# Optimization experiments

Hardware: AMD Instinct MI355X
Metric: run time of the kernel (lower is better)

Reference implementation:

```python
import jax, jax.numpy as jnp
import numpy as np
from jax import lax

SEQ, IN, H, L = 4096, 512, 2048, 2


def setup_inputs() -> dict:
    key = jax.random.key(0)
    ks = jax.random.split(key, 16)
    s = 1.0 / np.sqrt(H)  # PyTorch LSTM init scale U(-1/sqrt(H), 1/sqrt(H))
    u = lambda k, shape: jax.random.uniform(k, shape, jnp.float32, -s, s)
    return {
        "x": jax.random.normal(ks[0], (SEQ, IN), jnp.float32),
        # layer 0 (input_size -> H)
        "w_ih0": u(ks[1], (4 * H, IN)),
        "w_hh0": u(ks[2], (4 * H, H)),
        "b_ih0": u(ks[3], (4 * H,)),
        "b_hh0": u(ks[4], (4 * H,)),
        # layer 1 (H -> H)
        "w_ih1": u(ks[5], (4 * H, H)),
        "w_hh1": u(ks[6], (4 * H, H)),
        "b_ih1": u(ks[7], (4 * H,)),
        "b_hh1": u(ks[8], (4 * H,)),
        # heads: Linear(H, 1)
        "w_t": u(ks[9], (1, H)),
        "b_t": u(ks[10], (1,)),
        "w_f": u(ks[11], (1, H)),
        "b_f": u(ks[12], (1,)),
    }


def _lstm_layer(xs, w_ih, w_hh, b_ih, b_hh):
    """Single-direction LSTM over xs [T, D_in] with batch=1. PyTorch gate order i,f,g,o."""
    # Precompute input contribution for all timesteps: [T, 4H]
    gx = xs @ w_ih.T + b_ih + b_hh

    def step(carry, g_in):
        h, c = carry
        g = g_in + h @ w_hh.T  # [4H]
        i, f, gg, o = jnp.split(g, 4)
        i = jax.nn.sigmoid(i)
        f = jax.nn.sigmoid(f)
        gg = jnp.tanh(gg)
        o = jax.nn.sigmoid(o)
        c = f * c + i * gg
        h = o * jnp.tanh(c)
        return (h, c), h

    h0 = jnp.zeros((H,), xs.dtype)
    c0 = jnp.zeros((H,), xs.dtype)
    (hT, _), hs = lax.scan(step, (h0, c0), gx)
    return hs, hT  # hs: [T, H], hT: [H]


def reference(x, w_ih0, w_hh0, b_ih0, b_hh0, w_ih1, w_hh1, b_ih1, b_hh1,
              w_t, b_t, w_f, b_f):
    hs0, _ = _lstm_layer(x, w_ih0, w_hh0, b_ih0, b_hh0)
    _, hT = _lstm_layer(hs0, w_ih1, w_hh1, b_ih1, b_hh1)
    lstm_out = hT.reshape(1, 1, H)  # matches torch lstm_out of last step
    target_out = lstm_out @ w_t.T + b_t  # (1,1,1)
    feature_out = lstm_out @ w_f.T + b_f  # (1,1,1)
    return (target_out, feature_out)
```

## Files before the change

### kernel.cpp

```cpp
#include <hip/hip_runtime.h>

typedef __attribute__((ext_vector_type(4))) float f32x4;
typedef __attribute__((ext_vector_type(8))) short short8;
typedef __attribute__((ext_vector_type(2))) _Float16 half2v;
typedef unsigned int u32;
typedef unsigned short u16;
typedef unsigned long long u64;

#define T_SEQ 4096
#define HDIM  2048
#define GDIM  8192
#define INDIM 512
#define NBLK  256
#define FLAG_STRIDE 32

#if defined(__has_builtin)
#if __has_builtin(__builtin_amdgcn_fdot2)
#define HAS_FDOT2 1
#endif
#if __has_builtin(__builtin_amdgcn_exp2f)
#define EXP2F(x) __builtin_amdgcn_exp2f(x)
#endif
#endif
#ifndef HAS_FDOT2
#define HAS_FDOT2 0
#endif
#ifndef EXP2F
#define EXP2F(x) exp2f(x)
#endif

__device__ __forceinline__ u16 f2bf(float x) {
  u32 u = __float_as_uint(x);
  return (u16)((u + 0x7fffu + ((u >> 16) & 1u)) >> 16);
}
__device__ __forceinline__ u16 f2h(float x) {
  _Float16 h = (_Float16)x;
  return __builtin_bit_cast(unsigned short, h);
}
__device__ __forceinline__ float hlo(u32 u) {
  return (float)__builtin_bit_cast(_Float16, (unsigned short)(u & 0xffffu));
}
__device__ __forceinline__ float hhi(u32 u) {
  return (float)__builtin_bit_cast(_Float16, (unsigned short)(u >> 16));
}

__device__ __forceinline__ int aload(const int* p) {
  return __hip_atomic_load(p, __ATOMIC_RELAXED, __HIP_MEMORY_SCOPE_AGENT);
}
__device__ __forceinline__ void astore(int* p, int v) {
  __hip_atomic_store(p, v, __ATOMIC_RELAXED, __HIP_MEMORY_SCOPE_AGENT);
}
__device__ __forceinline__ u64 aload64(const u64* p) {
  return __hip_atomic_load(p, __ATOMIC_RELAXED, __HIP_MEMORY_SCOPE_AGENT);
}
__device__ __forceinline__ void astoref(float* p, float v) {
  __hip_atomic_store(p, v, __ATOMIC_RELAXED, __HIP_MEMORY_SCOPE_AGENT);
}

__global__ void k_zero_f32(float* __restrict__ p, int n) {
  int i = blockIdx.x * blockDim.x + threadIdx.x;
  int st = gridDim.x * blockDim.x;
  for (; i < n; i += st) p[i] = 0.f;
}

__global__ void k_bias_sum(const float* __restrict__ a, const float* __restrict__ b,
                           float* __restrict__ o, int n) {
  int i = blockIdx.x * blockDim.x + threadIdx.x;
  if (i < n) o[i] = a[i] + b[i];
}

__global__ void k_cvt_bf16(const float* __restrict__ in, u16* __restrict__ out, int n) {
  int i = blockIdx.x * blockDim.x + threadIdx.x;
  int st = gridDim.x * blockDim.x;
  for (; i < n; i += st) out[i] = f2bf(in[i]);
}

__global__ __launch_bounds__(512) void k_prep_whh(const float* __restrict__ w,
                                                  uint4* __restrict__ out) {
  const int bid = blockIdx.x;
  const int tid = threadIdx.x;
#pragma unroll
  for (int s = 0; s < 16; ++s) {
    int slot = s * 512 + tid;
    int l = slot & 63, r3 = slot >> 6;
    int g = r3 & 3, q = (r3 >> 2) & 3, wv = r3 >> 4;
    int grow = q * HDIM + bid * 8 + wv;
    const float* src = w + (size_t)grow * HDIM + l * 32 + g * 8;
    uint4 o;
    o.x = (u32)f2h(src[0]) | ((u32)f2h(src[1]) << 16);
    o.y = (u32)f2h(src[2]) | ((u32)f2h(src[3]) << 16);
    o.z = (u32)f2h(src[4]) | ((u32)f2h(src[5]) << 16);
    o.w = (u32)f2h(src[6]) | ((u32)f2h(src[7]) << 16);
    out[((size_t)bid * 16 + s) * 512 + tid] = o;
  }
}

template <bool AF32>
__global__ __launch_bounds__(256) void gemm_bt_bias(
    const void* __restrict__ Av, const u16* __restrict__ B,
    const float* __restrict__ bias, float* __restrict__ C,
    int M, int N, int K)
{
  __shared__ u16 As[128 * 64];
  __shared__ u16 Bs[128 * 64];
  const int tid = threadIdx.x;
  const int m0 = blockIdx.y * 128;
  const int n0 = blockIdx.x * 128;
  const int w = tid >> 6;
  const int lane = tid & 63;
  const int wm = (w >> 1) * 64, wn = (w & 1) * 64;
  const int lr = lane & 15, lk = lane >> 4;

  f32x4 acc[4][4];
  f32x4 zero = {0.f, 0.f, 0.f, 0.f};
#pragma unroll
  for (int i = 0; i < 4; ++i)
#pragma unroll
    for (int j = 0; j < 4; ++j) acc[i][j] = zero;

  const int r = tid >> 1;
  const int sbase = (tid & 1) * 4;

  for (int kt = 0; kt < K; kt += 64) {
    uint4 va[4], vb[4];
#pragma unroll
    for (int s = 0; s < 4; ++s) {
      if constexpr (AF32) {
        const float* ga = (const float*)Av + (size_t)(m0 + r) * K + kt + (sbase + s) * 8;
        float4 f0 = *reinterpret_cast<const float4*>(ga);
        float4 f1 = *reinterpret_cast<const float4*>(ga + 4);
        va[s].x = (u32)f2bf(f0.x) | ((u32)f2bf(f0.y) << 16);
        va[s].y = (u32)f2bf(f0.z) | ((u32)f2bf(f0.w) << 16);
        va[s].z = (u32)f2bf(f1.x) | ((u32)f2bf(f1.y) << 16);
        va[s].w = (u32)f2bf(f1.z) | ((u32)f2bf(f1.w) << 16);
      } else {
        const u16* ga = (const u16*)Av + (size_t)(m0 + r) * K + kt + (sbase + s) * 8;
        va[s] = *reinterpret_cast<const uint4*>(ga);
      }
      const u16* gb = B + (size_t)(n0 + r) * K + kt + (sbase + s) * 8;
      vb[s] = *reinterpret_cast<const uint4*>(gb);
    }
    __syncthreads();
#pragma unroll
    for (int s = 0; s < 4; ++s) {
      int ps = (sbase + s) ^ (r & 7);
      *reinterpret_cast<uint4*>(&As[r * 64 + ps * 8]) = va[s];
      *reinterpret_cast<uint4*>(&Bs[r * 64 + ps * 8]) = vb[s];
    }
    __syncthreads();
#pragma unroll
    for (int k32 = 0; k32 < 2; ++k32) {
      short8 af[4], bg[4];
#pragma unroll
      for (int i = 0; i < 4; ++i) {
        int arow = wm + i * 16 + lr;
        int aslot = (k32 * 4 + lk) ^ (arow & 7);
        af[i] = *reinterpret_cast<const short8*>(&As[arow * 64 + aslot * 8]);
        int brow = wn + i * 16 + lr;
        int bslot = (k32 * 4 + lk) ^ (brow & 7);
        bg[i] = *reinterpret_cast<const short8*>(&Bs[brow * 64 + bslot * 8]);
      }
#pragma unroll
      for (int i = 0; i < 4; ++i)
#pragma unroll
        for (int j = 0; j < 4; ++j)
          acc[i][j] = __builtin_amdgcn_mfma_f32_16x16x32_bf16(af[i], bg[j], acc[i][j], 0, 0, 0);
    }
  }

#pragma unroll
  for (int j = 0; j < 4; ++j) {
    int gcol = n0 + wn + j * 16 + lr;
    float bv = bias[gcol];
#pragma unroll
    for (int i = 0; i < 4; ++i) {
      int grow = m0 + wm + i * 16 + lk * 4;
#pragma unroll
      for (int rr = 0; rr < 4; ++rr)
        C[(size_t)(grow + rr) * N + gcol] = acc[i][j][rr] + bv;
    }
  }
}

__global__ __launch_bounds__(512, 1) void lstm_rec(
    const float* __restrict__ gx,
    const uint4* __restrict__ wp,
    float* __restrict__ hhist,
    int* __restrict__ flags,
    int hmask, int T)
{
  __shared__ uint4 wlds[16 * 512];
  __shared__ float4 hT[512];
  const int tid = threadIdx.x;
  const int bid = blockIdx.x;
  const int wv = tid >> 6;
  const int l = tid & 63;

#pragma unroll
  for (int s = 0; s < 16; ++s)
    wlds[s * 512 + tid] = wp[((size_t)bid * 16 + s) * 512 + tid];
  __syncthreads();

  float c = 0.f;

  for (int t = 0; t < T; ++t) {
    uint4 wr[16];
#pragma unroll
    for (int s = 0; s < 16; ++s) wr[s] = wlds[(wv * 16 + s) * 64 + l];
#pragma unroll
    for (int s = 0; s < 16; ++s)
      asm volatile("" : "+v"(wr[s].x), "+v"(wr[s].y), "+v"(wr[s].z), "+v"(wr[s].w));

    float gv = 0.f;
    if (l < 4) gv = gx[(size_t)t * GDIM + l * HDIM + bid * 8 + wv];

    if (wv == 0) {
      const int* f0 = &flags[(l * 4 + 0) * FLAG_STRIDE];
      const int* f1 = &flags[(l * 4 + 1) * FLAG_STRIDE];
      const int* f2 = &flags[(l * 4 + 2) * FLAG_STRIDE];
      const int* f3 = &flags[(l * 4 + 3) * FLAG_STRIDE];
      while (true) {
        int m0 = min(min(aload(f0), aload(f1)), min(aload(f2), aload(f3)));
        if (__all(m0 >= t)) break;
        __builtin_amdgcn_s_sleep(1);
      }
    }
    __syncthreads();

    {
      const u64* hsrc = (const u64*)(hhist + (size_t)(t & hmask) * HDIM);
      u64 d0 = aload64(&hsrc[tid * 2]);
      u64 d1 = aload64(&hsrc[tid * 2 + 1]);
      float4 hv;
      hv.x = __uint_as_float((u32)d0);
      hv.y = __uint_as_float((u32)(d0 >> 32));
      hv.z = __uint_as_float((u32)d1);
      hv.w = __uint_as_float((u32)(d1 >> 32));
      int G2 = tid & 7, sb = tid >> 3;
      hT[G2 * 64 + (sb ^ ((G2 * 9) & 63))] = hv;
    }
    __syncthreads();

    float a0 = 0.f, a1 = 0.f, a2 = 0.f, a3 = 0.f;
#pragma unroll
    for (int g = 0; g < 4; ++g) {
      const int G0 = g * 2, G1 = g * 2 + 1;
      float4 h0 = hT[G0 * 64 + (l ^ ((G0 * 9) & 63))];
      float4 h1 = hT[G1 * 64 + (l ^ ((G1 * 9) & 63))];
#if HAS_FDOT2
      half2v p0, p1, p2, p3;
      p0[0] = (_Float16)h0.x; p0[1] = (_Float16)h0.y;
      p1[0] = (_Float16)h0.z; p1[1] = (_Float16)h0.w;
      p2[0] = (_Float16)h1.x; p2[1] = (_Float16)h1.y;
      p3[0] = (_Float16)h1.z; p3[1] = (_Float16)h1.w;
#define FD2(wu, pp, acc) __builtin_amdgcn_fdot2(__builtin_bit_cast(half2v, (wu)), (pp), (acc), false)
      a0 = FD2(wr[0 + g].x, p0, FD2(wr[0 + g].y, p1, FD2(wr[0 + g].z, p2, FD2(wr[0 + g].w, p3, a0))));
      a1 = FD2(wr[4 + g].x, p0, FD2(wr[4 + g].y, p1, FD2(wr[4 + g].z, p2, FD2(wr[4 + g].w, p3, a1))));
      a2 = FD2(wr[8 + g].x, p0, FD2(wr[8 + g].y, p1, FD2(wr[8 + g].z, p2, FD2(wr[8 + g].w, p3, a2))));
      a3 = FD2(wr[12 + g].x, p0, FD2(wr[12 + g].y, p1, FD2(wr[12 + g].z, p2, FD2(wr[12 + g].w, p3, a3))));
#undef FD2
#else
      a0 += hlo(wr[0 + g].x) * h0.x + hhi(wr[0 + g].x) * h0.y + hlo(wr[0 + g].y) * h0.z + hhi(wr[0 + g].y) * h0.w +
            hlo(wr[0 + g].z) * h1.x + hhi(wr[0 + g].z) * h1.y + hlo(wr[0 + g].w) * h1.z + hhi(wr[0 + g].w) * h1.w;
      a1 += hlo(wr[4 + g].x) * h0.x + hhi(wr[4 + g].x) * h0.y + hlo(wr[4 + g].y) * h0.z + hhi(wr[4 + g].y) * h0.w +
            hlo(wr[4 + g].z) * h1.x + hhi(wr[4 + g].z) * h1.y + hlo(wr[4 + g].w) * h1.z + hhi(wr[4 + g].w) * h1.w;
      a2 += hlo(wr[8 + g].x) * h0.x + hhi(wr[8 + g].x) * h0.y + hlo(wr[8 + g].y) * h0.z + hhi(wr[8 + g].y) * h0.w +
            hlo(wr[8 + g].z) * h1.x + hhi(wr[8 + g].z) * h1.y + hlo(wr[8 + g].w) * h1.z + hhi(wr[8 + g].w) * h1.w;
      a3 += hlo(wr[12 + g].x) * h0.x + hhi(wr[12 + g].x) * h0.y + hlo(wr[12 + g].y) * h0.z + hhi(wr[12 + g].y) * h0.w +
            hlo(wr[12 + g].z) * h1.x + hhi(wr[12 + g].z) * h1.y + hlo(wr[12 + g].w) * h1.z + hhi(wr[12 + g].w) * h1.w;
#endif
    }
#pragma unroll
    for (int m = 32; m >= 1; m >>= 1) {
      a0 += __shfl_xor(a0, m);
      a1 += __shfl_xor(a1, m);
      a2 += __shfl_xor(a2, m);
      a3 += __shfl_xor(a3, m);
    }
    float g0 = __shfl(gv, 0), g1 = __shfl(gv, 1), g2 = __shfl(gv, 2), g3 = __shfl(gv, 3);

    {
      const float L2E = 1.44269504f;
      float pre = (l & 2) ? ((l & 1) ? a3 + g3 : a2 + g2)
                          : ((l & 1) ? a1 + g1 : a0 + g0);
      float k = (l == 2) ? 2.f * L2E : -L2E;
      float e = EXP2F(k * pre);
      float act = (l == 2) ? (1.f - 2.f / (e + 1.f)) : (1.f / (1.f + e));
      float i_ = __shfl(act, 0);
      float f_ = __shfl(act, 1);
      float gg = __shfl(act, 2);
      float o_ = __shfl(act, 3);
      c = f_ * c + i_ * gg;
      float th = 1.f - 2.f / (EXP2F(2.f * L2E * c) + 1.f);
      float hval = o_ * th;
      if (l == 0) {
        astoref(&hhist[(size_t)((t + 1) & hmask) * HDIM + bid * 8 + wv], hval);
      }
    }
    __syncthreads();
    if (tid == 0) astore(&flags[bid * FLAG_STRIDE], t + 1);
  }
}

__global__ void k_heads(const float* __restrict__ h, const float* __restrict__ wt,
                        const float* __restrict__ bt, const float* __restrict__ wf,
                        const float* __restrict__ bfp, float* __restrict__ out) {
  int tid = threadIdx.x;
  float st = 0.f, sf = 0.f;
  for (int i = tid; i < HDIM; i += 256) {
    float hv = h[i];
    st += hv * wt[i];
    sf += hv * wf[i];
  }
#pragma unroll
  for (int m = 32; m >= 1; m >>= 1) {
    st += __shfl_xor(st, m, 64);
    sf += __shfl_xor(sf, m, 64);
  }
  __shared__ float ra[4], rb[4];
  if ((tid & 63) == 0) { ra[tid >> 6] = st; rb[tid >> 6] = sf; }
  __syncthreads();
  if (tid == 0) {
    out[0] = ra[0] + ra[1] + ra[2] + ra[3] + bt[0];
    out[1] = rb[0] + rb[1] + rb[2] + rb[3] + bfp[0];
  }
}

extern "C" void kernel_launch(void* const* d_in, const int* in_sizes, int n_in,
                              void* d_out, int out_size, void* d_ws, size_t ws_size,
                              hipStream_t stream) {
  const float* x     = (const float*)d_in[0];
  const float* w_ih0 = (const float*)d_in[1];
  const float* w_hh0 = (const float*)d_in[2];
  const float* b_ih0 = (const float*)d_in[3];
  const float* b_hh0 = (const float*)d_in[4];
  const float* w_ih1 = (const float*)d_in[5];
  const float* w_hh1 = (const float*)d_in[6];
  const float* b_ih1 = (const float*)d_in[7];
  const float* b_hh1 = (const float*)d_in[8];
  const float* w_t   = (const float*)d_in[9];
  const float* b_t   = (const float*)d_in[10];
  const float* w_f   = (const float*)d_in[11];
  const float* b_f   = (const float*)d_in[12];

  char* p = (char*)d_ws;
  float* gx    = (float*)(p);
  float* hs0f  = (float*)(p + 134217728);
  u16*   xb    = (u16*)  (p + 167780352);
  u16*   wb0   = (u16*)  (p + 171974656);
  u16*   wb1   = (u16*)  (p + 180363264);
  uint4* wprep = (uint4*)(p + 213917696);
  float* h1r   = (float*)(p + 247472128);
  float* bias0 = (float*)(p + 247504896);
  float* bias1 = (float*)(p + 247537664);
  int*   flags0= (int*)  (p + 247570432);
  int*   flags1= (int*)  (p + 247603200);

  k_zero_f32<<<8, 256, 0, stream>>>(hs0f, HDIM);
  k_zero_f32<<<32, 256, 0, stream>>>(h1r, 4 * HDIM);
  k_zero_f32<<<64, 256, 0, stream>>>((float*)flags0, 2 * NBLK * FLAG_STRIDE);
  k_bias_sum<<<GDIM / 256, 256, 0, stream>>>(b_ih0, b_hh0, bias0, GDIM);
  k_bias_sum<<<GDIM / 256, 256, 0, stream>>>(b_ih1, b_hh1, bias1, GDIM);
  k_cvt_bf16<<<1024, 256, 0, stream>>>(x, xb, T_SEQ * INDIM);
  k_cvt_bf16<<<1024, 256, 0, stream>>>(w_ih0, wb0, GDIM * INDIM);
  k_cvt_bf16<<<2048, 256, 0, stream>>>(w_ih1, wb1, GDIM * HDIM);

  k_prep_whh<<<NBLK, 512, 0, stream>>>(w_hh0, wprep);
  gemm_bt_bias<false><<<dim3(GDIM / 128, T_SEQ / 128), 256, 0, stream>>>(
      xb, wb0, bias0, gx, T_SEQ, GDIM, INDIM);
  lstm_rec<<<NBLK, 512, 0, stream>>>(gx, wprep, hs0f, flags0, 0x7fffffff, T_SEQ);

  gemm_bt_bias<true><<<dim3(GDIM / 128, T_SEQ / 128), 256, 0, stream>>>(
      hs0f + HDIM, wb1, bias1, gx, T_SEQ, GDIM, HDIM);
  k_prep_whh<<<NBLK, 512, 0, stream>>>(w_hh1, wprep);
  lstm_rec<<<NBLK, 512, 0, stream>>>(gx, wprep, h1r, flags1, 3, T_SEQ);

  k_heads<<<1, 256, 0, stream>>>(h1r + (size_t)(T_SEQ & 3) * HDIM, w_t, b_t, w_f, b_f,
                                 (float*)d_out);
}
```

Measured before the change: 23.56 ms.

## Replace flag-based step barrier with tagged h publication in low mantissa bits

Removes the separate per-block flag store and poll followed by a second h load. Each block now publishes its hidden values into a 4-slot ring, one cache line per block, with a 2-bit epoch tag stored in the low mantissa bits of each float. Consumers spin directly on the data until the tags match, so the wait and the data fetch become a single round trip. LDS h buffers are double-buffered, which lets one __syncthreads per step be dropped. The cost is a tiny precision loss in h from overwriting mantissa bits, plus more polling traffic from wave 0.

```diff
diff --git a/kernel.cpp b/kernel.cpp
--- a/kernel.cpp
+++ b/kernel.cpp
@@ -12,7 +12,7 @@
 #define GDIM  8192
 #define INDIM 512
 #define NBLK  256
-#define FLAG_STRIDE 32
+#define LINE_U64 16
 
 #if defined(__has_builtin)
 #if __has_builtin(__builtin_amdgcn_fdot2)
@@ -44,23 +44,29 @@
   return (float)__builtin_bit_cast(_Float16, (unsigned short)(u >> 16));
 }
 
-__device__ __forceinline__ int aload(const int* p) {
-  return __hip_atomic_load(p, __ATOMIC_RELAXED, __HIP_MEMORY_SCOPE_AGENT);
-}
-__device__ __forceinline__ void astore(int* p, int v) {
-  __hip_atomic_store(p, v, __ATOMIC_RELAXED, __HIP_MEMORY_SCOPE_AGENT);
-}
 __device__ __forceinline__ u64 aload64(const u64* p) {
   return __hip_atomic_load(p, __ATOMIC_RELAXED, __HIP_MEMORY_SCOPE_AGENT);
 }
-__device__ __forceinline__ void astoref(float* p, float v) {
+__device__ __forceinline__ void astore64(u64* p, u64 v) {
   __hip_atomic_store(p, v, __ATOMIC_RELAXED, __HIP_MEMORY_SCOPE_AGENT);
+}
+__device__ __forceinline__ bool tagok(u64 x, u32 tg) {
+  return (((u32)x & 3u) == tg) && (((u32)(x >> 32) & 3u) == tg);
 }
 
 __global__ void k_zero_f32(float* __restrict__ p, int n) {
   int i = blockIdx.x * blockDim.x + threadIdx.x;
   int st = gridDim.x * blockDim.x;
   for (; i < n; i += st) p[i] = 0.f;
+}
+
+__global__ void k_init_hpub(u64* __restrict__ a, u64* __restrict__ b) {
+  int i = blockIdx.x * blockDim.x + threadIdx.x;
+  if (i < 4 * NBLK * LINE_U64) {
+    u64 v = (i < NBLK * LINE_U64) ? 0x0000000100000001ULL : 0ULL;
+    a[i] = v;
+    b[i] = v;
+  }
 }
 
 __global__ void k_bias_sum(const float* __restrict__ a, const float* __restrict__ b,
@@ -182,15 +188,18 @@
   }
 }
 
-__global__ __launch_bounds__(512, 1) void lstm_rec(
+__global__ __launch_bounds__(512, 1)
+__attribute__((amdgpu_waves_per_eu(2, 2)))
+void lstm_rec(
     const float* __restrict__ gx,
     const uint4* __restrict__ wp,
-    float* __restrict__ hhist,
-    int* __restrict__ flags,
-    int hmask, int T)
+    u64* __restrict__ hpub,
+    float* __restrict__ hist,
+    int T)
 {
   __shared__ uint4 wlds[16 * 512];
-  __shared__ float4 hT[512];
+  __shared__ float4 hT2[2][512];
+  __shared__ float h_out[8];
   const int tid = threadIdx.x;
   const int bid = blockIdx.x;
   const int wv = tid >> 6;
@@ -215,29 +224,37 @@
     if (l < 4) gv = gx[(size_t)t * GDIM + l * HDIM + bid * 8 + wv];
 
     if (wv == 0) {
-      const int* f0 = &flags[(l * 4 + 0) * FLAG_STRIDE];
-      const int* f1 = &flags[(l * 4 + 1) * FLAG_STRIDE];
-      const int* f2 = &flags[(l * 4 + 2) * FLAG_STRIDE];
-      const int* f3 = &flags[(l * 4 + 3) * FLAG_STRIDE];
-      while (true) {
-        int m0 = min(min(aload(f0), aload(f1)), min(aload(f2), aload(f3)));
-        if (__all(m0 >= t)) break;
-        __builtin_amdgcn_s_sleep(1);
+      const u32 tg = (((u32)t >> 2) + 1) & 3u;
+      const u64* base = hpub + (size_t)(t & 3) * (NBLK * LINE_U64);
+      u64 d[16];
+      u32 done = 0;
+      while (done != 0xFu) {
+#pragma unroll
+        for (int pi = 0; pi < 4; ++pi) {
+          if (done & (1u << pi)) continue;
+          const u64* ln = base + (size_t)(l * 4 + pi) * LINE_U64;
+          u64 x0 = aload64(ln + 0);
+          u64 x1 = aload64(ln + 1);
+          u64 x2 = aload64(ln + 2);
+          u64 x3 = aload64(ln + 3);
+          if (tagok(x0, tg) && tagok(x1, tg) && tagok(x2, tg) && tagok(x3, tg)) {
+            d[pi * 4 + 0] = x0; d[pi * 4 + 1] = x1;
+            d[pi * 4 + 2] = x2; d[pi * 4 + 3] = x3;
+            done |= (1u << pi);
+          }
+        }
+        if (done != 0xFu) __builtin_amdgcn_s_sleep(1);
       }
-    }
-    __syncthreads();
-
-    {
-      const u64* hsrc = (const u64*)(hhist + (size_t)(t & hmask) * HDIM);
-      u64 d0 = aload64(&hsrc[tid * 2]);
-      u64 d1 = aload64(&hsrc[tid * 2 + 1]);
-      float4 hv;
-      hv.x = __uint_as_float((u32)d0);
-      hv.y = __uint_as_float((u32)(d0 >> 32));
-      hv.z = __uint_as_float((u32)d1);
-      hv.w = __uint_as_float((u32)(d1 >> 32));
-      int G2 = tid & 7, sb = tid >> 3;
-      hT[G2 * 64 + (sb ^ ((G2 * 9) & 63))] = hv;
+#pragma unroll
+      for (int j = 0; j < 8; ++j) {
+        u64 a = d[2 * j], b = d[2 * j + 1];
+        float4 hv;
+        hv.x = __uint_as_float((u32)a);
+        hv.y = __uint_as_float((u32)(a >> 32));
+        hv.z = __uint_as_float((u32)b);
+        hv.w = __uint_as_float((u32)(b >> 32));
+        hT2[t & 1][j * 64 + (l ^ ((j * 9) & 63))] = hv;
+      }
     }
     __syncthreads();
 
@@ -245,8 +262,8 @@
 #pragma unroll
     for (int g = 0; g < 4; ++g) {
       const int G0 = g * 2, G1 = g * 2 + 1;
-      float4 h0 = hT[G0 * 64 + (l ^ ((G0 * 9) & 63))];
-      float4 h1 = hT[G1 * 64 + (l ^ ((G1 * 9) & 63))];
+      float4 h0 = hT2[t & 1][G0 * 64 + (l ^ ((G0 * 9) & 63))];
+      float4 h1 = hT2[t & 1][G1 * 64 + (l ^ ((G1 * 9) & 63))];
 #if HAS_FDOT2
       half2v p0, p1, p2, p3;
       p0[0] = (_Float16)h0.x; p0[1] = (_Float16)h0.y;
@@ -292,23 +309,34 @@
       float o_ = __shfl(act, 3);
       c = f_ * c + i_ * gg;
       float th = 1.f - 2.f / (EXP2F(2.f * L2E * c) + 1.f);
-      float hval = o_ * th;
-      if (l == 0) {
-        astoref(&hhist[(size_t)((t + 1) & hmask) * HDIM + bid * 8 + wv], hval);
+      if (l == 0) h_out[wv] = o_ * th;
+    }
+    __syncthreads();
+
+    if (wv == 4 && l < 4) {
+      const u32 tg1 = (((u32)(t + 1) >> 2) + 1) & 3u;
+      float ha = h_out[2 * l], hb = h_out[2 * l + 1];
+      u32 ba = (__float_as_uint(ha) & ~3u) | tg1;
+      u32 bb = (__float_as_uint(hb) & ~3u) | tg1;
+      astore64(hpub + (size_t)((t + 1) & 3) * (NBLK * LINE_U64) + bid * LINE_U64 + l,
+               (u64)ba | ((u64)bb << 32));
+      if (hist) {
+        float2 hv2; hv2.x = ha; hv2.y = hb;
+        *reinterpret_cast<float2*>(hist + (size_t)(t + 1) * HDIM + bid * 8 + 2 * l) = hv2;
       }
     }
-    __syncthreads();
-    if (tid == 0) astore(&flags[bid * FLAG_STRIDE], t + 1);
-  }
-}
-
-__global__ void k_heads(const float* __restrict__ h, const float* __restrict__ wt,
+  }
+}
+
+__global__ void k_heads(const u64* __restrict__ hp, const float* __restrict__ wt,
                         const float* __restrict__ bt, const float* __restrict__ wf,
                         const float* __restrict__ bfp, float* __restrict__ out) {
   int tid = threadIdx.x;
   float st = 0.f, sf = 0.f;
   for (int i = tid; i < HDIM; i += 256) {
-    float hv = h[i];
+    u64 wpair = hp[(size_t)(i >> 3) * LINE_U64 + ((i & 7) >> 1)];
+    float hv = (i & 1) ? __uint_as_float((u32)(wpair >> 32))
+                       : __uint_as_float((u32)wpair);
     st += hv * wt[i];
     sf += hv * wf[i];
   }
@@ -350,15 +378,13 @@
   u16*   wb0   = (u16*)  (p + 171974656);
   u16*   wb1   = (u16*)  (p + 180363264);
   uint4* wprep = (uint4*)(p + 213917696);
-  float* h1r   = (float*)(p + 247472128);
-  float* bias0 = (float*)(p + 247504896);
-  float* bias1 = (float*)(p + 247537664);
-  int*   flags0= (int*)  (p + 247570432);
-  int*   flags1= (int*)  (p + 247603200);
+  u64*   hpub0 = (u64*)  (p + 247472128);
+  u64*   hpub1 = (u64*)  (p + 247603200);
+  float* bias0 = (float*)(p + 247734272);
+  float* bias1 = (float*)(p + 247767040);
 
   k_zero_f32<<<8, 256, 0, stream>>>(hs0f, HDIM);
-  k_zero_f32<<<32, 256, 0, stream>>>(h1r, 4 * HDIM);
-  k_zero_f32<<<64, 256, 0, stream>>>((float*)flags0, 2 * NBLK * FLAG_STRIDE);
+  k_init_hpub<<<64, 256, 0, stream>>>(hpub0, hpub1);
   k_bias_sum<<<GDIM / 256, 256, 0, stream>>>(b_ih0, b_hh0, bias0, GDIM);
   k_bias_sum<<<GDIM / 256, 256, 0, stream>>>(b_ih1, b_hh1, bias1, GDIM);
   k_cvt_bf16<<<1024, 256, 0, stream>>>(x, xb, T_SEQ * INDIM);
@@ -368,13 +394,13 @@
   k_prep_whh<<<NBLK, 512, 0, stream>>>(w_hh0, wprep);
   gemm_bt_bias<false><<<dim3(GDIM / 128, T_SEQ / 128), 256, 0, stream>>>(
       xb, wb0, bias0, gx, T_SEQ, GDIM, INDIM);
-  lstm_rec<<<NBLK, 512, 0, stream>>>(gx, wprep, hs0f, flags0, 0x7fffffff, T_SEQ);
+  lstm_rec<<<NBLK, 512, 0, stream>>>(gx, wprep, hpub0, hs0f, T_SEQ);
 
   gemm_bt_bias<true><<<dim3(GDIM / 128, T_SEQ / 128), 256, 0, stream>>>(
       hs0f + HDIM, wb1, bias1, gx, T_SEQ, GDIM, HDIM);
   k_prep_whh<<<NBLK, 512, 0, stream>>>(w_hh1, wprep);
-  lstm_rec<<<NBLK, 512, 0, stream>>>(gx, wprep, h1r, flags1, 3, T_SEQ);
-
-  k_heads<<<1, 256, 0, stream>>>(h1r + (size_t)(T_SEQ & 3) * HDIM, w_t, b_t, w_f, b_f,
-                                 (float*)d_out);
-}
+  lstm_rec<<<NBLK, 512, 0, stream>>>(gx, wprep, hpub1, (float*)nullptr, T_SEQ);
+
+  k_heads<<<1, 256, 0, stream>>>(hpub1 + (size_t)(T_SEQ & 3) * (NBLK * LINE_U64),
+                                 w_t, b_t, w_f, b_f, (float*)d_out);
+}
```

Result: slower. 35.12 ms (+49.1%).

## Replace per-block flag barrier with per-wave byte flags in LSTM recurrence

Applied to the files above, without the earlier changes.

Each wave now publishes its own readiness byte, an 8-bit step tag, right after storing its h value, with a waitcnt before the byte store. This removes the trailing __syncthreads and the single-thread flag store at the end of every step. Waiters poll 64-bit words and accept a byte equal to either t or t+1, using a zero-byte bit trick. For layer 0 it also adds an sc0/sc1 cache-bypassing dwordx4 load of the hidden state. The aim is to shorten the critical path of the per-timestep cross-block handshake, at the cost of inline asm and wraparound-tag reasoning.

```diff
diff --git a/kernel.cpp b/kernel.cpp
--- a/kernel.cpp
+++ b/kernel.cpp
@@ -3,8 +3,10 @@
 typedef __attribute__((ext_vector_type(4))) float f32x4;
 typedef __attribute__((ext_vector_type(8))) short short8;
 typedef __attribute__((ext_vector_type(2))) _Float16 half2v;
+typedef __attribute__((ext_vector_type(4))) unsigned int u32x4;
 typedef unsigned int u32;
 typedef unsigned short u16;
+typedef unsigned char u8;
 typedef unsigned long long u64;
 
 #define T_SEQ 4096
@@ -12,7 +14,7 @@
 #define GDIM  8192
 #define INDIM 512
 #define NBLK  256
-#define FLAG_STRIDE 32
+#define FLAG_LINE 128
 
 #if defined(__has_builtin)
 #if __has_builtin(__builtin_amdgcn_fdot2)
@@ -44,17 +46,15 @@
   return (float)__builtin_bit_cast(_Float16, (unsigned short)(u >> 16));
 }
 
-__device__ __forceinline__ int aload(const int* p) {
-  return __hip_atomic_load(p, __ATOMIC_RELAXED, __HIP_MEMORY_SCOPE_AGENT);
-}
-__device__ __forceinline__ void astore(int* p, int v) {
-  __hip_atomic_store(p, v, __ATOMIC_RELAXED, __HIP_MEMORY_SCOPE_AGENT);
-}
 __device__ __forceinline__ u64 aload64(const u64* p) {
   return __hip_atomic_load(p, __ATOMIC_RELAXED, __HIP_MEMORY_SCOPE_AGENT);
 }
 __device__ __forceinline__ void astoref(float* p, float v) {
   __hip_atomic_store(p, v, __ATOMIC_RELAXED, __HIP_MEMORY_SCOPE_AGENT);
+}
+
+__device__ __forceinline__ u64 zbytes(u64 v) {
+  return (v - 0x0101010101010101ULL) & ~v & 0x8080808080808080ULL;
 }
 
 __global__ void k_zero_f32(float* __restrict__ p, int n) {
@@ -186,8 +186,8 @@
     const float* __restrict__ gx,
     const uint4* __restrict__ wp,
     float* __restrict__ hhist,
-    int* __restrict__ flags,
-    int hmask, int T)
+    u8* __restrict__ flagb,
+    int hmask, int sc_fetch, int T)
 {
   __shared__ uint4 wlds[16 * 512];
   __shared__ float4 hT[512];
@@ -215,27 +215,45 @@
     if (l < 4) gv = gx[(size_t)t * GDIM + l * HDIM + bid * 8 + wv];
 
     if (wv == 0) {
-      const int* f0 = &flags[(l * 4 + 0) * FLAG_STRIDE];
-      const int* f1 = &flags[(l * 4 + 1) * FLAG_STRIDE];
-      const int* f2 = &flags[(l * 4 + 2) * FLAG_STRIDE];
-      const int* f3 = &flags[(l * 4 + 3) * FLAG_STRIDE];
+      const u64 rt  = 0x0101010101010101ULL * (u64)((u32)t & 0xFF);
+      const u64 rt1 = 0x0101010101010101ULL * (u64)((u32)(t + 1) & 0xFF);
+      const u64* f0 = (const u64*)(flagb + (size_t)(l * 4 + 0) * FLAG_LINE);
+      const u64* f1 = (const u64*)(flagb + (size_t)(l * 4 + 1) * FLAG_LINE);
+      const u64* f2 = (const u64*)(flagb + (size_t)(l * 4 + 2) * FLAG_LINE);
+      const u64* f3 = (const u64*)(flagb + (size_t)(l * 4 + 3) * FLAG_LINE);
+      const u64 ALL = 0x8080808080808080ULL;
       while (true) {
-        int m0 = min(min(aload(f0), aload(f1)), min(aload(f2), aload(f3)));
-        if (__all(m0 >= t)) break;
+        u64 x0 = aload64(f0), x1 = aload64(f1), x2 = aload64(f2), x3 = aload64(f3);
+        bool ok = ((zbytes(x0 ^ rt) | zbytes(x0 ^ rt1)) == ALL) &&
+                  ((zbytes(x1 ^ rt) | zbytes(x1 ^ rt1)) == ALL) &&
+                  ((zbytes(x2 ^ rt) | zbytes(x2 ^ rt1)) == ALL) &&
+                  ((zbytes(x3 ^ rt) | zbytes(x3 ^ rt1)) == ALL);
+        if (__all(ok)) break;
         __builtin_amdgcn_s_sleep(1);
       }
     }
     __syncthreads();
 
     {
-      const u64* hsrc = (const u64*)(hhist + (size_t)(t & hmask) * HDIM);
-      u64 d0 = aload64(&hsrc[tid * 2]);
-      u64 d1 = aload64(&hsrc[tid * 2 + 1]);
+      const float* hp = hhist + (size_t)(t & hmask) * HDIM + tid * 4;
       float4 hv;
-      hv.x = __uint_as_float((u32)d0);
-      hv.y = __uint_as_float((u32)(d0 >> 32));
-      hv.z = __uint_as_float((u32)d1);
-      hv.w = __uint_as_float((u32)(d1 >> 32));
+      if (sc_fetch) {
+        u32x4 hu;
+        asm volatile("global_load_dwordx4 %0, %1, off sc0 sc1\n\ts_waitcnt vmcnt(0)"
+                     : "=v"(hu) : "v"(hp) : "memory");
+        hv.x = __uint_as_float(hu.x);
+        hv.y = __uint_as_float(hu.y);
+        hv.z = __uint_as_float(hu.z);
+        hv.w = __uint_as_float(hu.w);
+      } else {
+        const u64* hsrc = (const u64*)hp;
+        u64 d0 = aload64(&hsrc[0]);
+        u64 d1 = aload64(&hsrc[1]);
+        hv.x = __uint_as_float((u32)d0);
+        hv.y = __uint_as_float((u32)(d0 >> 32));
+        hv.z = __uint_as_float((u32)d1);
+        hv.w = __uint_as_float((u32)(d1 >> 32));
+      }
       int G2 = tid & 7, sb = tid >> 3;
       hT[G2 * 64 + (sb ^ ((G2 * 9) & 63))] = hv;
     }
@@ -292,13 +310,15 @@
       float o_ = __shfl(act, 3);
       c = f_ * c + i_ * gg;
       float th = 1.f - 2.f / (EXP2F(2.f * L2E * c) + 1.f);
-      float hval = o_ * th;
       if (l == 0) {
-        astoref(&hhist[(size_t)((t + 1) & hmask) * HDIM + bid * 8 + wv], hval);
+        astoref(&hhist[(size_t)((t + 1) & hmask) * HDIM + bid * 8 + wv],
+                o_ * th);
+        u8* fp = flagb + (size_t)bid * FLAG_LINE + wv;
+        u32 tag = (u32)(t + 1) & 0xFF;
+        asm volatile("s_waitcnt vmcnt(0)\n\tglobal_store_byte %0, %1, off sc0 sc1"
+                     :: "v"(fp), "v"(tag) : "memory");
       }
     }
-    __syncthreads();
-    if (tid == 0) astore(&flags[bid * FLAG_STRIDE], t + 1);
   }
 }
 
@@ -353,12 +373,12 @@
   float* h1r   = (float*)(p + 247472128);
   float* bias0 = (float*)(p + 247504896);
   float* bias1 = (float*)(p + 247537664);
-  int*   flags0= (int*)  (p + 247570432);
-  int*   flags1= (int*)  (p + 247603200);
+  u8*    flags0b = (u8*) (p + 247570432);
+  u8*    flags1b = (u8*) (p + 247603200);
 
   k_zero_f32<<<8, 256, 0, stream>>>(hs0f, HDIM);
   k_zero_f32<<<32, 256, 0, stream>>>(h1r, 4 * HDIM);
-  k_zero_f32<<<64, 256, 0, stream>>>((float*)flags0, 2 * NBLK * FLAG_STRIDE);
+  k_zero_f32<<<64, 256, 0, stream>>>((float*)flags0b, 2 * 8192);
   k_bias_sum<<<GDIM / 256, 256, 0, stream>>>(b_ih0, b_hh0, bias0, GDIM);
   k_bias_sum<<<GDIM / 256, 256, 0, stream>>>(b_ih1, b_hh1, bias1, GDIM);
   k_cvt_bf16<<<1024, 256, 0, stream>>>(x, xb, T_SEQ * INDIM);
@@ -368,12 +388,13 @@
   k_prep_whh<<<NBLK, 512, 0, stream>>>(w_hh0, wprep);
   gemm_bt_bias<false><<<dim3(GDIM / 128, T_SEQ / 128), 256, 0, stream>>>(
       xb, wb0, bias0, gx, T_SEQ, GDIM, INDIM);
-  lstm_rec<<<NBLK, 512, 0, stream>>>(gx, wprep, hs0f, flags0, 0x7fffffff, T_SEQ);
+  lstm_rec<<<NBLK, 512, 0, stream>>>(gx, wprep, hs0f, flags0b,
+                                     0x7fffffff, 1, T_SEQ);
 
   gemm_bt_bias<true><<<dim3(GDIM / 128, T_SEQ / 128), 256, 0, stream>>>(
       hs0f + HDIM, wb1, bias1, gx, T_SEQ, GDIM, HDIM);
   k_prep_whh<<<NBLK, 512, 0, stream>>>(w_hh1, wprep);
-  lstm_rec<<<NBLK, 512, 0, stream>>>(gx, wprep, h1r, flags1, 3, T_SEQ);
+  lstm_rec<<<NBLK, 512, 0, stream>>>(gx, wprep, h1r, flags1b, 3, 0, T_SEQ);
 
   k_heads<<<1, 256, 0, stream>>>(h1r + (size_t)(T_SEQ & 3) * HDIM, w_t, b_t, w_f, b_f,
                                  (float*)d_out);
```

Result: slower. 43.32 ms (+83.9%).
